# Kernel optimization log

Measured on AMD Instinct MI355X. Metric: run time of the kernel, lower is better.

## Reference

```python
import jax, jax.numpy as jnp
import numpy as np


def setup_inputs() -> dict:
    key = jax.random.key(0)
    n_symbols, code_length = 2, 16
    n_types, batch_size = 256, 128
    n_all = n_symbols ** code_length  # 65536 codes
    # enumerate full binary code space as one-hot [A, L, S]
    bits = (np.arange(n_all)[:, None] >> np.arange(code_length - 1, -1, -1)) & 1
    all_codes = np.eye(n_symbols, dtype=np.float32)[bits]
    # source distribution, sorted descending (abundant words first), normalized
    pi = jax.random.uniform(key, (n_types,), dtype=jnp.float32) + 0.1
    pi = jnp.sort(pi)[::-1]
    pi = pi / pi.sum()
    return {
        "pi_t": pi,
        "all_codes_als": jnp.asarray(all_codes),
        "code_length": code_length,
        "n_types": n_types,
        "batch_size": batch_size,
        "two_body_max_n_interactions": 32,
        "top_proposals_per_column": 1024,
        "random_proposals_per_column": 256,
    }


def reference(pi_t, all_codes_als, code_length, n_types, batch_size,
              two_body_max_n_interactions, top_proposals_per_column,
              random_proposals_per_column):
    A, L, S = all_codes_als.shape
    B, T = batch_size, n_types
    P = min(top_proposals_per_column, A)
    R = min(random_proposals_per_column, A)
    W = min(two_body_max_n_interactions, T - 1)  # 'earlier' dropout window
    dt = pi_t.dtype
    base_key = jax.random.key(42)

    # one-body potential: abundance-weighted quadratic on code hamming weight
    w_a = all_codes_als[:, :, 1].sum(-1)  # [A] hamming weight of each code
    type_rank_t = jnp.arange(T, dtype=dt) / T

    def one_body(pi, type_rank):
        target = code_length * (1.0 - type_rank)
        return pi * (w_a - target) ** 2 / code_length  # [A]

    win_off = jnp.arange(W)

    def step(c_btls, i_p):
        i_t = i_p  # sweep_order is identity
        ob_a = one_body(pi_t[i_t], type_rank_t[i_t])
        # top proposals by lowest one-body energy + random proposals (fixed K)
        _, top_idx = jax.lax.top_k(-ob_a, P)
        kr = jax.random.fold_in(base_key, i_p)
        k_rand, k_samp = jax.random.split(kr)
        rand_idx = jax.random.randint(k_rand, (R,), 0, A)
        idx_k = jnp.concatenate([top_idx, rand_idx])  # [K = P + R]
        codes_kls = all_codes_als[idx_k]               # [K, L, S]
        ob_k = ob_a[idx_k]                             # [K]
        # two-body over fixed window of up to W previous columns ('earlier')
        win = i_p - W + win_off                        # [W] previous columns
        valid = (win >= 0).astype(dt)
        win_c = jnp.clip(win, 0, T - 1)
        c2_bwls = jnp.take(c_btls, win_c, axis=1)      # [B, W, L, S]
        overlap_bkw = jnp.einsum('kls,bwls->bkw', codes_kls, c2_bwls)
        pi_w = pi_t[win_c] * valid                     # [W]
        tb_bk = pi_t[i_t] * (overlap_bkw * pi_w[None, None, :]).sum(-1)
        i_pf = i_p.astype(dt)
        n_int = jnp.minimum(i_pf, jnp.asarray(W, dt))
        factor = jnp.where(i_pf > 0, i_pf / jnp.maximum(n_int, 1.0), 0.0)
        two_body_bk = factor * tb_bk                   # dropout compensation
        unnorm_bk = -(ob_k[None, :] + two_body_bk)     # [B, K]
        log_prob_bk = jax.nn.log_softmax(unnorm_bk, axis=-1)
        # action_policy == 'sampled'
        c_b = jax.random.categorical(k_samp, log_prob_bk, axis=-1)  # [B]
        c_btls = c_btls.at[:, i_t].set(codes_kls[c_b])
        lp_b = jnp.take_along_axis(log_prob_bk, c_b[:, None], axis=-1)[:, 0]
        return c_btls, lp_b

    c0 = jnp.zeros((B, T, L, S), dtype=dt)
    c_btls, lp_tb = jax.lax.scan(step, c0, jnp.arange(T))
    log_prob_b = lp_tb.mean(0)  # mean over columns, matching torch cat+mean
    return c_btls, log_prob_b
```

## Files before the change

### kernel.cpp

```cpp
#include <hip/hip_runtime.h>
#include <stdint.h>
#include <math.h>


#define JAX_PARTITIONABLE 1

#define T_COLS 256
#define B_ROWS 128
#define KC     1280
#define PTOP   1024
#define RRAND  256
#define WWIN   32
#define NCAND  20
#define NWAVES 4
#define NGW    8
#define NTHR   ((NWAVES + NGW) * 64)
#define NCPL   5
#define BLOCK_S 1024
#define NWAVE_S (BLOCK_S / 64)

__device__ __constant__ int dC[17][17] = {
  {1},
  {1,1},
  {1,2,1},
  {1,3,3,1},
  {1,4,6,4,1},
  {1,5,10,10,5,1},
  {1,6,15,20,15,6,1},
  {1,7,21,35,35,21,7,1},
  {1,8,28,56,70,56,28,8,1},
  {1,9,36,84,126,126,84,36,9,1},
  {1,10,45,120,210,252,210,120,45,10,1},
  {1,11,55,165,330,462,462,330,165,55,11,1},
  {1,12,66,220,495,792,924,792,495,220,66,12,1},
  {1,13,78,286,715,1287,1716,1716,1287,715,286,78,13,1},
  {1,14,91,364,1001,2002,3003,3432,3003,2002,1001,364,91,14,1},
  {1,15,105,455,1365,3003,5005,6435,6435,5005,3003,1365,455,105,15,1},
  {1,16,120,560,1820,4368,8008,11440,12870,11440,8008,4368,1820,560,120,16,1}
};

__device__ __forceinline__ void tf_block(uint32_t k0, uint32_t k1,
                                         uint32_t x0, uint32_t x1,
                                         uint32_t& o0, uint32_t& o1) {
  uint32_t ks2 = k0 ^ k1 ^ 0x1BD11BDAu;
  x0 += k0; x1 += k1;
#define TFR(r) { x0 += x1; x1 = (x1 << (r)) | (x1 >> (32 - (r))); x1 ^= x0; }
  TFR(13) TFR(15) TFR(26) TFR(6)   x0 += k1;  x1 += ks2 + 1u;
  TFR(17) TFR(29) TFR(16) TFR(24)  x0 += ks2; x1 += k0 + 2u;
  TFR(13) TFR(15) TFR(26) TFR(6)   x0 += k0;  x1 += k1 + 3u;
  TFR(17) TFR(29) TFR(16) TFR(24)  x0 += k1;  x1 += ks2 + 4u;
  TFR(13) TFR(15) TFR(26) TFR(6)   x0 += ks2; x1 += k0 + 5u;
#undef TFR
  o0 = x0; o1 = x1;
}

__device__ __forceinline__ void derive_keys(int step,
                                            uint32_t* krand, uint32_t* ksamp,
                                            uint32_t* k2) {
  uint32_t y0, y1;
  tf_block(0u, 42u, 0u, (uint32_t)step, y0, y1);
  uint32_t kr0 = y0, kr1 = y1;
#if JAX_PARTITIONABLE
  uint32_t r0, r1;
  tf_block(kr0, kr1, 0u, 0u, r0, r1);
  if (krand) { krand[0] = r0; krand[1] = r1; }
  if (ksamp) { tf_block(kr0, kr1, 0u, 1u, y0, y1); ksamp[0] = y0; ksamp[1] = y1; }
  if (k2)    { tf_block(r0, r1, 0u, 1u, y0, y1);  k2[0] = y0;  k2[1] = y1; }
#else
  uint32_t a0,a1,b0,b1;
  tf_block(kr0, kr1, 0u, 2u, a0, a1);
  tf_block(kr0, kr1, 1u, 3u, b0, b1);
  if (krand) { krand[0] = a0; krand[1] = b0; }
  if (ksamp) { ksamp[0] = a1; ksamp[1] = b1; }
  if (k2) {
    uint32_t c0,c1,d0,d1;
    tf_block(a0, b0, 0u, 2u, c0, c1);
    tf_block(a0, b0, 1u, 3u, d0, d1);
    k2[0] = c1; k2[1] = d1;
  }
#endif
}

__device__ __forceinline__ float gumbel_from_bits(uint32_t bits) {
  uint32_t fb = (bits >> 9) | 0x3f800000u;
  float f = __uint_as_float(fb) - 1.0f;
  float u = (f == 0.0f) ? 1.17549435e-38f : f;
  float l1 = (float)log((double)u);
  float l2 = (float)log((double)(-l1));
  return -l2;
}

__device__ __forceinline__ float gumbel_at(uint32_t ks0, uint32_t ks1, uint32_t j) {
  uint32_t g0, g1;
#if JAX_PARTITIONABLE
  tf_block(ks0, ks1, 0u, j, g0, g1);
  return gumbel_from_bits(g0 ^ g1);
#else
  uint32_t half = (uint32_t)(B_ROWS * KC / 2);
  if (j < half) { tf_block(ks0, ks1, j, j + half, g0, g1);  return gumbel_from_bits(g0); }
  else          { tf_block(ks0, ks1, j - half, j, g0, g1);  return gumbel_from_bits(g1); }
#endif
}

__global__ void __launch_bounds__(256)
cand_kernel(unsigned short* __restrict__ candg) {
  const int step = blockIdx.x;
  const int tid  = threadIdx.x;
  __shared__ int s_dC[17][17];
  __shared__ int s_gw0[17], s_gw1[17], s_gbase[17];
  __shared__ int s_ngrp;
  __shared__ uint32_t s_k2[2];
  for (int i = tid; i < 289; i += 256) s_dC[i/17][i%17] = dC[i/17][i%17];
  if (tid == 0) {
    uint32_t k2[2];
    derive_keys(step, nullptr, nullptr, k2);
    s_k2[0] = k2[0]; s_k2[1] = k2[1];
    int ws[17], am[17];
    for (int w = 0; w < 17; ++w) {
      int m = 16 * w - 256 + step;
      am[w] = m < 0 ? -m : m;
      ws[w] = w;
    }
    for (int a2 = 1; a2 < 17; ++a2) {
      int wv = ws[a2], kv = am[wv];
      int j2 = a2 - 1;
      while (j2 >= 0 && am[ws[j2]] > kv) { ws[j2 + 1] = ws[j2]; --j2; }
      ws[j2 + 1] = wv;
    }
    int ng = 0, base = 0, idx = 0;
    while (idx < 17) {
      int w0 = ws[idx]; int a0v = am[w0]; int w1 = -1;
      if (idx + 1 < 17 && am[ws[idx + 1]] == a0v) { w1 = ws[idx + 1]; ++idx; }
      ++idx;
      s_gw0[ng] = w0; s_gw1[ng] = w1; s_gbase[ng] = base;
      base += dC[16][w0] + (w1 >= 0 ? dC[16][w1] : 0);
      ++ng;
      if (base >= PTOP) break;
    }
    s_ngrp = ng;
  }
  __syncthreads();
  for (int p = tid; p < PTOP; p += 256) {
    int g = 0;
    for (int t2 = 1; t2 < s_ngrp; ++t2) if (s_gbase[t2] <= p) g = t2;
    int q  = p - s_gbase[g];
    int r0 = s_gw0[g], r1 = s_gw1[g];
    uint32_t code = 0;
    for (int pos = 15; pos >= 0; --pos) {
      int n0 = ((r0 >= 0 && r0 <= pos) ? s_dC[pos][r0] : 0)
             + ((r1 >= 0 && r1 <= pos) ? s_dC[pos][r1] : 0);
      if (q >= n0) { q -= n0; code |= (1u << pos); --r0; if (r1 >= 0) --r1; }
    }
    candg[step * KC + p] = (unsigned short)code;
  }
  {
    int t2 = tid;
    uint32_t a0, a1;
#if JAX_PARTITIONABLE
    tf_block(s_k2[0], s_k2[1], 0u, (uint32_t)t2, a0, a1);
    candg[step * KC + PTOP + t2] = (unsigned short)((a0 ^ a1) & 0xFFFFu);
#else
    if (t2 < 128) { tf_block(s_k2[0], s_k2[1], (uint32_t)t2, (uint32_t)(128 + t2), a0, a1);
                    candg[step * KC + PTOP + t2] = (unsigned short)(a0 & 0xFFFFu); }
    else          { tf_block(s_k2[0], s_k2[1], (uint32_t)(t2 - 128), (uint32_t)t2, a0, a1);
                    candg[step * KC + PTOP + t2] = (unsigned short)(a1 & 0xFFFFu); }
#endif
  }
}

__device__ __forceinline__ unsigned pl_down32_u(unsigned x) {
  unsigned d = x, s = x;
  asm volatile("s_nop 1\n\tv_permlane32_swap_b32 %0, %1" : "+v"(d), "+v"(s));
  return s;
}
__device__ __forceinline__ unsigned pl_down16_u(unsigned x) {
  unsigned d = x, s = x;
  asm volatile("s_nop 1\n\tv_permlane16_swap_b32 %0, %1" : "+v"(d), "+v"(s));
  return s;
}
template<int N>
__device__ __forceinline__ unsigned dpp_shl_u(unsigned x) {
  return (unsigned)__builtin_amdgcn_update_dpp(0, (int)x, 0x100 | N, 0xF, 0xF, true);
}
__device__ __forceinline__ float pl_down32_f(float x) {
  return __uint_as_float(pl_down32_u(__float_as_uint(x)));
}
__device__ __forceinline__ float pl_down16_f(float x) {
  return __uint_as_float(pl_down16_u(__float_as_uint(x)));
}
template<int N>
__device__ __forceinline__ float dpp_shl_f(float x) {
  return __uint_as_float(dpp_shl_u<N>(__float_as_uint(x)));
}
__device__ __forceinline__ double pl_down32_d(double x) {
  unsigned lo = pl_down32_u((unsigned)__double2loint(x));
  unsigned hi = pl_down32_u((unsigned)__double2hiint(x));
  return __hiloint2double((int)hi, (int)lo);
}
__device__ __forceinline__ double pl_down16_d(double x) {
  unsigned lo = pl_down16_u((unsigned)__double2loint(x));
  unsigned hi = pl_down16_u((unsigned)__double2hiint(x));
  return __hiloint2double((int)hi, (int)lo);
}
template<int N>
__device__ __forceinline__ double dpp_shl_d(double x) {
  unsigned lo = dpp_shl_u<N>((unsigned)__double2loint(x));
  unsigned hi = dpp_shl_u<N>((unsigned)__double2hiint(x));
  return __hiloint2double((int)hi, (int)lo);
}
__device__ __forceinline__ float bcast0_f(float x) {
  return __uint_as_float((unsigned)__builtin_amdgcn_readfirstlane((int)__float_as_uint(x)));
}
__device__ __forceinline__ int bcast0_i(int x) {
  return __builtin_amdgcn_readfirstlane(x);
}
__device__ __forceinline__ double bcast0_d(double x) {
  int lo = __builtin_amdgcn_readfirstlane(__double2loint(x));
  int hi = __builtin_amdgcn_readfirstlane(__double2hiint(x));
  return __hiloint2double(hi, lo);
}

#define LGKM_BAR()                                                            \
  do {                                                                        \
    asm volatile("s_waitcnt lgkmcnt(0)" ::: "memory");                        \
    __builtin_amdgcn_s_barrier();                                             \
  } while (0)

#define STEP_F(S, CUR, CC, CN)                                                \
  if (wid < NWAVES) {                                                         \
    const int step = (S);                                                     \
        \
    float GGl[NCPL];                                                          \
    _Pragma("unroll")                                                         \
    for (int i = 0; i < NCPL; ++i)                                            \
      GGl[i] = s_gg[CUR][(NCPL * wid + i) * 64 + lane];                       \
                                   \
    const int sn = (step + 1 < T_COLS) ? step + 1 : step;                     \
    _Pragma("unroll")                                                         \
    for (int i = 0; i < NCPL; ++i)                                            \
      CN[i] = candg[sn * KC + (NCPL * wid + i) * 64 + lane];                  \
             \
    if (lane < 16) {                                                          \
      if (step > 0) {                                                         \
        double pw = (double)s_pi[step - 1];                                   \
        if ((c_last >> lane) & 1u) p1_d += pw;                                \
        pt_d += pw;                                                           \
      }                                                                       \
      if (step >= 33) {                                                       \
        double pw = (double)s_pi[step - 33];                                  \
        if (((uint32_t)s_cint[step - 33] >> lane) & 1u) p1_d -= pw;           \
        pt_d -= pw;                                                           \
      }                                                                       \
    }                                                                         \
    float Dl = (float)(pt_d - (p1_d + p1_d));                                 \
    double s0d = p1_d;                                                        \
    s0d += dpp_shl_d<1>(s0d);                                                 \
    s0d += dpp_shl_d<2>(s0d);                                                 \
    s0d += dpp_shl_d<4>(s0d);                                                 \
    s0d += dpp_shl_d<8>(s0d);                                                 \
    const float S0f  = bcast0_f((float)s0d);                                  \
    const float Pt16 = bcast0_f((float)(16.0 * pt_d));                        \
    {                                                                         \
      int n = lane >> 4, v = lane & 15;                                       \
      float d0 = __shfl(Dl, 4 * n + 0);                                       \
      float d1 = __shfl(Dl, 4 * n + 1);                                       \
      float d2 = __shfl(Dl, 4 * n + 2);                                       \
      float d3 = __shfl(Dl, 4 * n + 3);                                       \
      float t = 0.0f;                                                         \
      if (v & 1) t += d0;                                                     \
      if (v & 2) t += d1;                                                     \
      if (v & 4) t += d2;                                                     \
      if (v & 8) t += d3;                                                     \
      s_T[n][v] = t;                                                          \
    }                                                                         \
    __builtin_amdgcn_wave_barrier();                                          \
    const float pi_i   = s_pi[step];                                          \
    const float i_pf   = (float)step;                                         \
    const float factor = (step > 0) ? (i_pf / fminf(i_pf, 32.0f)) : 0.0f;     \
    float un[NCPL];                                                           \
    _Pragma("unroll")                                                         \
    for (int i = 0; i < NCPL; ++i) {                                          \
      uint32_t c = CC[i];                                                     \
      float sc = S0f + s_T[0][c & 15];                                        \
      sc += s_T[1][(c >> 4) & 15];                                            \
      sc += s_T[2][(c >> 8) & 15];                                            \
      sc += s_T[3][(c >> 12) & 15];                                           \
      float sv = Pt16 - sc;                                                   \
      int w = __popc(c);                                                      \
      int m = 16 * w - 256 + step;                                            \
      float sq  = (float)(m * m) * 0.00390625f;                               \
      float obk = (pi_i * sq) * 0.0625f;                                      \
      un[i] = -(obk + factor * (pi_i * sv));                                  \
    }                                                                         \
    float wmw = fmaxf(fmaxf(fmaxf(un[0], un[1]), fmaxf(un[2], un[3])),        \
                      un[4]);                                                 \
    s_cf[wid][lane] = wmw;                                                    \
    LGKM_BAR();                                                               \
    float wm = fmaxf(fmaxf(s_cf[0][lane], s_cf[1][lane]),                     \
                     fmaxf(s_cf[2][lane], s_cf[3][lane]));                    \
    wm = fmaxf(wm, pl_down32_f(wm));                                          \
    wm = fmaxf(wm, pl_down16_f(wm));                                          \
    wm = fmaxf(wm, dpp_shl_f<8>(wm));                                         \
    wm = fmaxf(wm, dpp_shl_f<4>(wm));                                         \
    wm = fmaxf(wm, dpp_shl_f<2>(wm));                                         \
    wm = fmaxf(wm, dpp_shl_f<1>(wm));                                         \
    wm = bcast0_f(wm);                                                        \
    double a0 = 0.0, a1 = 0.0;                                                \
    _Pragma("unroll")                                                         \
    for (int i = 0; i < NCPL; ++i) {                                          \
      float e = expf(un[i] - wm);                                             \
      if ((NCPL * wid + i) & 1) a1 += (double)e; else a0 += (double)e;        \
    }                                                                         \
    s_cd[wid][lane] = a0 + a1;                                                \
    LGKM_BAR();                                                               \
    double sw = ((s_cd[0][lane] + s_cd[1][lane]) + s_cd[2][lane])             \
                + s_cd[3][lane];                                              \
    sw += pl_down32_d(sw);                                                    \
    sw += pl_down16_d(sw);                                                    \
    sw += dpp_shl_d<8>(sw);                                                   \
    sw += dpp_shl_d<4>(sw);                                                   \
    sw += dpp_shl_d<2>(sw);                                                   \
    sw += dpp_shl_d<1>(sw);                                                   \
    const float lsum = logf((float)bcast0_d(sw));                             \
    float bz; int bi; float bu;                                               \
    {                                                                         \
      bz = ((un[0] - wm) - lsum) + GGl[0];                                    \
      bi = ((64 * (NCPL * wid) + lane) << 16) | (int)CC[0];                   \
      bu = un[0];                                                             \
      _Pragma("unroll")                                                       \
      for (int i = 1; i < NCPL; ++i) {                                        \
        float zi = ((un[i] - wm) - lsum) + GGl[i];                            \
        int   ii = ((64 * (NCPL * wid + i) + lane) << 16) | (int)CC[i];       \
        if (zi > bz || (zi == bz && ii < bi)) { bz = zi; bi = ii; bu = un[i]; }\
      }                                                                       \
    }                                                                         \
    s_cz[wid][lane] = bz; s_ci[wid][lane] = bi; s_cu[wid][lane] = bu;         \
    LGKM_BAR();                                                               \
    bz = s_cz[0][lane]; bi = s_ci[0][lane]; bu = s_cu[0][lane];               \
    _Pragma("unroll")                                                         \
    for (int w = 1; w < NWAVES; ++w) {                                        \
      float oz = s_cz[w][lane]; int oi = s_ci[w][lane];                       \
      float ou = s_cu[w][lane];                                               \
      if (oz > bz || (oz == bz && oi < bi)) { bz = oz; bi = oi; bu = ou; }    \
    }                                                                         \
    {                                                                         \
      float oz = pl_down32_f(bz); int oi = (int)pl_down32_u((unsigned)bi);    \
      float ou = pl_down32_f(bu);                                             \
      if (oz > bz || (oz == bz && oi < bi)) { bz = oz; bi = oi; bu = ou; }    \
    }                                                                         \
    {                                                                         \
      float oz = pl_down16_f(bz); int oi = (int)pl_down16_u((unsigned)bi);    \
      float ou = pl_down16_f(bu);                                             \
      if (oz > bz || (oz == bz && oi < bi)) { bz = oz; bi = oi; bu = ou; }    \
    }                                                                         \
    {                                                                         \
      float oz = dpp_shl_f<8>(bz); int oi = (int)dpp_shl_u<8>((unsigned)bi);  \
      float ou = dpp_shl_f<8>(bu);                                            \
      if (oz > bz || (oz == bz && oi < bi)) { bz = oz; bi = oi; bu = ou; }    \
    }                                                                         \
    {                                                                         \
      float oz = dpp_shl_f<4>(bz); int oi = (int)dpp_shl_u<4>((unsigned)bi);  \
      float ou = dpp_shl_f<4>(bu);                                            \
      if (oz > bz || (oz == bz && oi < bi)) { bz = oz; bi = oi; bu = ou; }    \
    }                                                                         \
    {                                                                         \
      float oz = dpp_shl_f<2>(bz); int oi = (int)dpp_shl_u<2>((unsigned)bi);  \
      float ou = dpp_shl_f<2>(bu);                                            \
      if (oz > bz || (oz == bz && oi < bi)) { bz = oz; bi = oi; bu = ou; }    \
    }                                                                         \
    {                                                                         \
      float oz = dpp_shl_f<1>(bz); int oi = (int)dpp_shl_u<1>((unsigned)bi);  \
      float ou = dpp_shl_f<1>(bu);                                            \
      if (oz > bz || (oz == bz && oi < bi)) { bz = oz; bi = oi; bu = ou; }    \
    }                                                                         \
    int wpk = bcast0_i(bi);                                                   \
    c_last = (uint32_t)wpk & 0xFFFFu;                                         \
    if (wid == 0 && lane == 0) {                                              \
      s_cint[step] = (unsigned short)c_last;                                  \
      lp_acc += (double)((bu - wm) - lsum);                                   \
    }                                                                         \
  } else {                                                                    \
                                                       \
    const int SN = (S) + 1;                                                   \
    const int ggl = (wid - NWAVES) * 64 + lane;                   \
    if (SN < T_COLS) {                                                        \
      const uint32_t k0 = s_ks[SN][0], k1 = s_ks[SN][1];                      \
      s_gg[1 - (CUR)][ggl] = gumbel_at(k0, k1, (uint32_t)(b * KC + ggl));     \
    }                                                                         \
    LGKM_BAR();                                                               \
    if (SN < T_COLS) {                                                        \
      const uint32_t k0 = s_ks[SN][0], k1 = s_ks[SN][1];                      \
      int k = 512 + ggl;                                                      \
      s_gg[1 - (CUR)][k] = gumbel_at(k0, k1, (uint32_t)(b * KC + k));         \
    }                                                                         \
    LGKM_BAR();                                                               \
    if (SN < T_COLS && ggl < 256) {                                           \
      const uint32_t k0 = s_ks[SN][0], k1 = s_ks[SN][1];                      \
      int k = 1024 + ggl;                                                     \
      s_gg[1 - (CUR)][k] = gumbel_at(k0, k1, (uint32_t)(b * KC + k));         \
    }                                                                         \
    LGKM_BAR();                                                               \
  }

__global__ void __launch_bounds__(NTHR, 1)
mrf_fused12(const float* __restrict__ pi, float* __restrict__ out,
            const unsigned short* __restrict__ candg) {
#pragma clang fp contract(off)
  const int b    = blockIdx.x;
  const int tid  = threadIdx.x;
  const int lane = tid & 63;
  const int wid  = tid >> 6;

  __shared__ float          s_pi[T_COLS];
  __shared__ unsigned short s_cint[T_COLS];
  __shared__ float          s_T[4][16];
  __shared__ float          s_cf[NWAVES][64];
  __shared__ double         s_cd[NWAVES][64];
  __shared__ float          s_cz[NWAVES][64];
  __shared__ int            s_ci[NWAVES][64];
  __shared__ float          s_cu[NWAVES][64];
  __shared__ float          s_gg[2][KC];
  __shared__ uint32_t       s_ks[T_COLS][2];

  for (int t = tid; t < T_COLS; t += NTHR) s_pi[t] = pi[t];
  if (tid < T_COLS) {
    uint32_t ks[2];
    derive_keys(tid, nullptr, ks, nullptr);
    s_ks[tid][0] = ks[0]; s_ks[tid][1] = ks[1];
  }
  __syncthreads();

  if (wid < NWAVES) __builtin_amdgcn_s_setprio(1);
  else              __builtin_amdgcn_s_setprio(0);

  double lp_acc = 0.0;
  uint32_t c_last = 0;
  double p1_d = 0.0, pt_d = 0.0;

  uint32_t cA[NCPL], cB[NCPL];

  if (wid >= NWAVES) {
    const int ggl = (wid - NWAVES) * 64 + lane;
    const uint32_t k0 = s_ks[0][0], k1 = s_ks[0][1];
    s_gg[0][ggl]       = gumbel_at(k0, k1, (uint32_t)(b * KC + ggl));
    s_gg[0][512 + ggl] = gumbel_at(k0, k1, (uint32_t)(b * KC + 512 + ggl));
    if (ggl < 256)
      s_gg[0][1024 + ggl] = gumbel_at(k0, k1, (uint32_t)(b * KC + 1024 + ggl));
  } else {
#pragma unroll
    for (int i = 0; i < NCPL; ++i)
      cA[i] = candg[(NCPL * wid + i) * 64 + lane];
  }
  __syncthreads();

  for (int s2 = 0; s2 < T_COLS; s2 += 2) {
    STEP_F(s2,     0, cA, cB)
    STEP_F(s2 + 1, 1, cB, cA)
  }

  __syncthreads();
  for (int idx2 = tid; idx2 < T_COLS * 32; idx2 += NTHR) {
    int t    = idx2 >> 5;
    int rem  = idx2 & 31;
    int l    = rem >> 1;
    int sbit = rem & 1;
    uint32_t code = s_cint[t];
    int bit = (int)((code >> (15 - l)) & 1u);
    out[(size_t)b * 8192 + idx2] = (float)(sbit ? bit : (1 - bit));
  }
  if (tid == 0) {
    out[(size_t)B_ROWS * 8192 + b] = (float)(lp_acc / 256.0);
  }
}

template<int MODE>
__global__ void __launch_bounds__(BLOCK_S)
mrf_seq_kernel(const float* __restrict__ pi, float* __restrict__ out,
               const float* __restrict__ gw,
               const unsigned short* __restrict__ candg) {
#pragma clang fp contract(off)
  const int b    = blockIdx.x;
  const int tid  = threadIdx.x;
  const bool has1 = tid < (KC - BLOCK_S);

  __shared__ float          s_pi[T_COLS];
  __shared__ unsigned short s_cand[KC];
  __shared__ float          s_unnorm[KC];
  __shared__ unsigned short s_cint[T_COLS];
  __shared__ int            s_dC[17][17];
  __shared__ int            s_gw0[17], s_gw1[17], s_gbase[17];
  __shared__ int            s_ngrp;
  __shared__ uint32_t       s_keys[6];
  __shared__ float          s_pw[WWIN];
  __shared__ unsigned short s_wc[WWIN];
  __shared__ float          s_redf[NWAVE_S];
  __shared__ double         s_redd[NWAVE_S];
  __shared__ int            s_redi[NWAVE_S];
  __shared__ float          s_bcast[2];

  for (int t = tid; t < T_COLS; t += BLOCK_S) s_pi[t] = pi[t];
  if (MODE == 0) {
    for (int i = tid; i < 289; i += BLOCK_S) s_dC[i/17][i%17] = dC[i/17][i%17];
  }
  double lp_acc = 0.0;
  __syncthreads();

  for (int step = 0; step < T_COLS; ++step) {
    if (tid == 0) {
      if (MODE == 1) {
        uint32_t ks[2];
        derive_keys(step, nullptr, ks, nullptr);
        s_keys[2] = ks[0]; s_keys[3] = ks[1];
      } else {
        uint32_t ks[2], k2[2];
        derive_keys(step, nullptr, ks, k2);
        s_keys[2] = ks[0]; s_keys[3] = ks[1];
        s_keys[4] = k2[0]; s_keys[5] = k2[1];
        int ws[17], am[17];
        for (int w = 0; w < 17; ++w) {
          int m = 16 * w - 256 + step;
          am[w] = m < 0 ? -m : m;
          ws[w] = w;
        }
        for (int a2 = 1; a2 < 17; ++a2) {
          int wvv = ws[a2], kv = am[wvv];
          int j2 = a2 - 1;
          while (j2 >= 0 && am[ws[j2]] > kv) { ws[j2 + 1] = ws[j2]; --j2; }
          ws[j2 + 1] = wvv;
        }
        int ng = 0, base = 0, idx = 0;
        while (idx < 17) {
          int w0 = ws[idx]; int a0v = am[w0]; int w1 = -1;
          if (idx + 1 < 17 && am[ws[idx + 1]] == a0v) { w1 = ws[idx + 1]; ++idx; }
          ++idx;
          s_gw0[ng] = w0; s_gw1[ng] = w1; s_gbase[ng] = base;
          base += dC[16][w0] + (w1 >= 0 ? dC[16][w1] : 0);
          ++ng;
          if (base >= PTOP) break;
        }
        s_ngrp = ng;
      }
    }
    if (tid < WWIN) {
      int win = step - WWIN + tid;
      s_pw[tid] = (win >= 0) ? s_pi[win] : 0.0f;
      s_wc[tid] = (win >= 0) ? s_cint[win] : (unsigned short)0;
    }
    __syncthreads();

    uint32_t c0, c1 = 0;
    if (MODE >= 1) {
      c0 = candg[step * KC + tid];
      if (has1) c1 = candg[step * KC + BLOCK_S + tid];
    } else {
      {
        int p = tid;
        int g = 0;
        for (int t2 = 1; t2 < s_ngrp; ++t2) if (s_gbase[t2] <= p) g = t2;
        int q  = p - s_gbase[g];
        int r0 = s_gw0[g], r1 = s_gw1[g];
        uint32_t code = 0;
        for (int pos = 15; pos >= 0; --pos) {
          int n0 = ((r0 >= 0 && r0 <= pos) ? s_dC[pos][r0] : 0)
                 + ((r1 >= 0 && r1 <= pos) ? s_dC[pos][r1] : 0);
          if (q >= n0) { q -= n0; code |= (1u << pos); --r0; if (r1 >= 0) --r1; }
        }
        c0 = code;
      }
      if (has1) {
        int t2 = tid;
        uint32_t a0, a1;
#if JAX_PARTITIONABLE
        tf_block(s_keys[4], s_keys[5], 0u, (uint32_t)t2, a0, a1);
        c1 = (a0 ^ a1) & 0xFFFFu;
#else
        if (t2 < 128) { tf_block(s_keys[4], s_keys[5], (uint32_t)t2, (uint32_t)(128 + t2), a0, a1);
                        c1 = a0 & 0xFFFFu; }
        else          { tf_block(s_keys[4], s_keys[5], (uint32_t)(t2 - 128), (uint32_t)t2, a0, a1);
                        c1 = a1 & 0xFFFFu; }
#endif
      }
    }
    s_cand[tid] = (unsigned short)c0;
    if (has1) s_cand[BLOCK_S + tid] = (unsigned short)c1;

    const float pi_i   = s_pi[step];
    const float i_pf   = (float)step;
    const float factor = (step > 0) ? (i_pf / fminf(i_pf, 32.0f)) : 0.0f;

    float un0, un1 = -3.402823466e+38f;
    {
      int w = __popc(c0);
      int m = 16 * w - 256 + step;
      float sq  = (float)(m * m) * 0.00390625f;
      float obk = (pi_i * sq) * 0.0625f;
      float s = 0.0f;
      for (int w2 = 0; w2 < WWIN; ++w2) {
        float ov = (float)(16 - __popc(c0 ^ (uint32_t)s_wc[w2]));
        s = s + s_pw[w2] * ov;
      }
      un0 = -(obk + factor * (pi_i * s));
    }
    if (has1) {
      int w = __popc(c1);
      int m = 16 * w - 256 + step;
      float sq  = (float)(m * m) * 0.00390625f;
      float obk = (pi_i * sq) * 0.0625f;
      float s = 0.0f;
      for (int w2 = 0; w2 < WWIN; ++w2) {
        float ov = (float)(16 - __popc(c1 ^ (uint32_t)s_wc[w2]));
        s = s + s_pw[w2] * ov;
      }
      un1 = -(obk + factor * (pi_i * s));
    }
    s_unnorm[tid] = un0;
    if (has1) s_unnorm[BLOCK_S + tid] = un1;

    float g0v = 0.0f, g1v = 0.0f;
    {
      const uint32_t ks0 = s_keys[2], ks1 = s_keys[3];
      g0v = gumbel_at(ks0, ks1, (uint32_t)(b * KC + tid));
      if (has1) g1v = gumbel_at(ks0, ks1, (uint32_t)(b * KC + BLOCK_S + tid));
    }

    float pmax = has1 ? fmaxf(un0, un1) : un0;
    for (int off = 32; off > 0; off >>= 1) pmax = fmaxf(pmax, __shfl_down(pmax, off));
    if ((tid & 63) == 0) s_redf[tid >> 6] = pmax;
    __syncthreads();
    if (tid == 0) {
      float mm = s_redf[0];
      for (int w2 = 1; w2 < NWAVE_S; ++w2) mm = fmaxf(mm, s_redf[w2]);
      s_bcast[0] = mm;
    }
    __syncthreads();
    const float rmax = s_bcast[0];

    double acc = (double)((float)exp((double)(un0 - rmax)));
    if (has1) acc += (double)((float)exp((double)(un1 - rmax)));
    for (int off = 32; off > 0; off >>= 1) acc += __shfl_down(acc, off);
    if ((tid & 63) == 0) s_redd[tid >> 6] = acc;
    __syncthreads();
    if (tid == 0) {
      double ss = 0.0;
      for (int w2 = 0; w2 < NWAVE_S; ++w2) ss += s_redd[w2];
      float sum_f = (float)ss;
      s_bcast[1] = (float)log((double)sum_f);
    }
    __syncthreads();
    const float lsum = s_bcast[1];

    float bz = ((un0 - rmax) - lsum) + g0v;
    int   bi = tid;
    if (has1) {
      float z1 = ((un1 - rmax) - lsum) + g1v;
      if (z1 > bz) { bz = z1; bi = BLOCK_S + tid; }
    }
    for (int off = 32; off > 0; off >>= 1) {
      float oz = __shfl_down(bz, off);
      int   oi = __shfl_down(bi, off);
      if (oz > bz || (oz == bz && oi < bi)) { bz = oz; bi = oi; }
    }
    if ((tid & 63) == 0) { s_redf[tid >> 6] = bz; s_redi[tid >> 6] = bi; }
    __syncthreads();
    if (tid == 0) {
      float bz2 = s_redf[0]; int bi2 = s_redi[0];
      for (int w2 = 1; w2 < NWAVE_S; ++w2) {
        if (s_redf[w2] > bz2 || (s_redf[w2] == bz2 && s_redi[w2] < bi2)) {
          bz2 = s_redf[w2]; bi2 = s_redi[w2];
        }
      }
      s_cint[step] = s_cand[bi2];
      float lpw = (s_unnorm[bi2] - rmax) - lsum;
      lp_acc += (double)lpw;
    }
    __syncthreads();
  }

  for (int idx2 = tid; idx2 < T_COLS * 32; idx2 += BLOCK_S) {
    int t    = idx2 >> 5;
    int rem  = idx2 & 31;
    int l    = rem >> 1;
    int sbit = rem & 1;
    uint32_t code = s_cint[t];
    int bit = (int)((code >> (15 - l)) & 1u);
    out[(size_t)b * 8192 + idx2] = (float)(sbit ? bit : (1 - bit));
  }
  if (tid == 0) {
    out[(size_t)B_ROWS * 8192 + b] = (float)(lp_acc / 256.0);
  }
}

extern "C" void kernel_launch(void* const* d_in, const int* in_sizes, int n_in,
                              void* d_out, int out_size, void* d_ws, size_t ws_size,
                              hipStream_t stream) {
  const float* pi = (const float*)d_in[0];
  float* out = (float*)d_out;

  const size_t cand_bytes = (size_t)T_COLS * KC * sizeof(unsigned short);

  if (ws_size >= cand_bytes) {
    unsigned short* candg = (unsigned short*)d_ws;
    cand_kernel<<<dim3(T_COLS), dim3(256), 0, stream>>>(candg);
    mrf_fused12<<<dim3(B_ROWS), dim3(NTHR), 0, stream>>>(pi, out, candg);
  } else {
    mrf_seq_kernel<0><<<dim3(B_ROWS), dim3(BLOCK_S), 0, stream>>>(pi, out, nullptr, nullptr);
  }
}
```

Before: 835.3 us.

## Offload second-half Gumbel noise generation to helper blocks on idle CUs

Launches 128 extra producer blocks that precompute the Gumbel noise for columns 128-255 into a global workspace and set a per-row done flag. The main sequential blocks generate noise inline for the first half, then spin on the flag and load the precomputed noise for the second half. The aim is to move hash and log work off the main blocks' critical path onto otherwise idle compute units. In exchange it adds global memory traffic, a memset, and a dependence on producer and consumer blocks being resident at the same time; if they are not, the spin-wait could deadlock.

Measured after the change: 739.0 us, median of 2. 1.13x faster.

```diff
diff --git a/kernel.cpp b/kernel.cpp
--- a/kernel.cpp
+++ b/kernel.cpp
@@ -7,6 +7,7 @@
 
 #define T_COLS 256
 #define B_ROWS 128
+#define HALF   128
 #define KC     1280
 #define PTOP   1024
 #define RRAND  256
@@ -380,33 +381,55 @@
       lp_acc += (double)((bu - wm) - lsum);                                   \
     }                                                                         \
   } else {                                                                    \
-                                                       \
+            \
     const int SN = (S) + 1;                                                   \
     const int ggl = (wid - NWAVES) * 64 + lane;                   \
+    const bool ld = (gw2 != nullptr) && (SN >= HALF);                         \
     if (SN < T_COLS) {                                                        \
-      const uint32_t k0 = s_ks[SN][0], k1 = s_ks[SN][1];                      \
-      s_gg[1 - (CUR)][ggl] = gumbel_at(k0, k1, (uint32_t)(b * KC + ggl));     \
+      if (!ld) {                                                              \
+        const uint32_t k0 = s_ks[SN][0], k1 = s_ks[SN][1];                    \
+        s_gg[1 - (CUR)][ggl] = gumbel_at(k0, k1, (uint32_t)(b * KC + ggl));   \
+      } else {                                                                \
+        if (SN == HALF) {                                                     \
+          while (__hip_atomic_load(&done[b], __ATOMIC_ACQUIRE,                \
+                                   __HIP_MEMORY_SCOPE_AGENT) == 0)            \
+            __builtin_amdgcn_s_sleep(16);                                     \
+        }                                                                     \
+        s_gg[1 - (CUR)][ggl] =                                                \
+            gw2[((size_t)b * HALF + (SN - HALF)) * KC + ggl];                 \
+      }                                                                       \
     }                                                                         \
     LGKM_BAR();                                                               \
     if (SN < T_COLS) {                                                        \
-      const uint32_t k0 = s_ks[SN][0], k1 = s_ks[SN][1];                      \
       int k = 512 + ggl;                                                      \
-      s_gg[1 - (CUR)][k] = gumbel_at(k0, k1, (uint32_t)(b * KC + k));         \
+      if (!ld) {                                                              \
+        const uint32_t k0 = s_ks[SN][0], k1 = s_ks[SN][1];                    \
+        s_gg[1 - (CUR)][k] = gumbel_at(k0, k1, (uint32_t)(b * KC + k));       \
+      } else {                                                                \
+        s_gg[1 - (CUR)][k] =                                                  \
+            gw2[((size_t)b * HALF + (SN - HALF)) * KC + k];                   \
+      }                                                                       \
     }                                                                         \
     LGKM_BAR();                                                               \
     if (SN < T_COLS && ggl < 256) {                                           \
-      const uint32_t k0 = s_ks[SN][0], k1 = s_ks[SN][1];                      \
       int k = 1024 + ggl;                                                     \
-      s_gg[1 - (CUR)][k] = gumbel_at(k0, k1, (uint32_t)(b * KC + k));         \
+      if (!ld) {                                                              \
+        const uint32_t k0 = s_ks[SN][0], k1 = s_ks[SN][1];                    \
+        s_gg[1 - (CUR)][k] = gumbel_at(k0, k1, (uint32_t)(b * KC + k));       \
+      } else {                                                                \
+        s_gg[1 - (CUR)][k] =                                                  \
+            gw2[((size_t)b * HALF + (SN - HALF)) * KC + k];                   \
+      }                                                                       \
     }                                                                         \
     LGKM_BAR();                                                               \
   }
 
 __global__ void __launch_bounds__(NTHR, 1)
-mrf_fused12(const float* __restrict__ pi, float* __restrict__ out,
-            const unsigned short* __restrict__ candg) {
+mrf_hybrid(const float* __restrict__ pi, float* __restrict__ out,
+           const unsigned short* __restrict__ candg,
+           float* __restrict__ gw2, int* __restrict__ done) {
 #pragma clang fp contract(off)
-  const int b    = blockIdx.x;
+  const int bid  = blockIdx.x;
   const int tid  = threadIdx.x;
   const int lane = tid & 63;
   const int wid  = tid >> 6;
@@ -421,6 +444,31 @@
   __shared__ float          s_cu[NWAVES][64];
   __shared__ float          s_gg[2][KC];
   __shared__ uint32_t       s_ks[T_COLS][2];
+
+  if (bid >= B_ROWS) {
+    const int pb = bid - B_ROWS;
+    if (tid < T_COLS) {
+      uint32_t ks[2];
+      derive_keys(tid, nullptr, ks, nullptr);
+      s_ks[tid][0] = ks[0]; s_ks[tid][1] = ks[1];
+    }
+    __syncthreads();
+    for (int s = HALF; s < T_COLS; ++s) {
+      const uint32_t k0 = s_ks[s][0], k1 = s_ks[s][1];
+      for (int k = tid; k < KC; k += NTHR)
+        gw2[((size_t)pb * HALF + (s - HALF)) * KC + k] =
+            gumbel_at(k0, k1, (uint32_t)(pb * KC + k));
+    }
+    __syncthreads();
+    if (tid == 0) {
+      __threadfence();
+      __hip_atomic_store(&done[pb], 1, __ATOMIC_RELEASE,
+                         __HIP_MEMORY_SCOPE_AGENT);
+    }
+    return;
+  }
+
+  const int b = bid;
 
   for (int t = tid; t < T_COLS; t += NTHR) s_pi[t] = pi[t];
   if (tid < T_COLS) {
@@ -697,11 +745,24 @@
   float* out = (float*)d_out;
 
   const size_t cand_bytes = (size_t)T_COLS * KC * sizeof(unsigned short);
-
-  if (ws_size >= cand_bytes) {
+  const size_t done_off   = cand_bytes;
+  const size_t done_bytes = 1024;
+  const size_t gw2_off    = done_off + done_bytes;
+  const size_t gw2_bytes  = (size_t)B_ROWS * HALF * KC * sizeof(float);
+
+  if (ws_size >= gw2_off + gw2_bytes) {
+    unsigned short* candg = (unsigned short*)d_ws;
+    int*   done = (int*)((char*)d_ws + done_off);
+    float* gw2  = (float*)((char*)d_ws + gw2_off);
+    hipMemsetAsync(done, 0, done_bytes, stream);
+    cand_kernel<<<dim3(T_COLS), dim3(256), 0, stream>>>(candg);
+    mrf_hybrid<<<dim3(2 * B_ROWS), dim3(NTHR), 0, stream>>>(
+        pi, out, candg, gw2, done);
+  } else if (ws_size >= cand_bytes) {
     unsigned short* candg = (unsigned short*)d_ws;
     cand_kernel<<<dim3(T_COLS), dim3(256), 0, stream>>>(candg);
-    mrf_fused12<<<dim3(B_ROWS), dim3(NTHR), 0, stream>>>(pi, out, candg);
+    mrf_hybrid<<<dim3(B_ROWS), dim3(NTHR), 0, stream>>>(
+        pi, out, candg, nullptr, nullptr);
   } else {
     mrf_seq_kernel<0><<<dim3(B_ROWS), dim3(BLOCK_S), 0, stream>>>(pi, out, nullptr, nullptr);
   }
```
